# Optimization experiments

Measured on AMD Instinct MI355X. Metric: run time of the kernel, lower is better.

## Reference

```python
import jax, jax.numpy as jnp
import numpy as np

D, LEN_IN, LEN_OUT = 2, 1, 10
H1, H2 = 32, 32
B, T = 4096, 512
F_IN = D * LEN_IN          # 2
F_OUT = D * LEN_OUT        # 20


def setup_inputs() -> dict:
    key = jax.random.key(0)
    ks = jax.random.split(key, 12)
    s = 1.0 / np.sqrt(H1)  # PyTorch default init scale for LSTMCell/Linear
    u = lambda k, shape: jax.random.uniform(k, shape, jnp.float32, -s, s)
    return {
        "x": jax.random.normal(ks[0], (B, T, F_IN), jnp.float32),
        # LSTMCell 1 (input 2 -> hidden 32); gate order i,f,g,o stacked on dim 0
        "W_ih1": u(ks[1], (4 * H1, F_IN)),
        "W_hh1": u(ks[2], (4 * H1, H1)),
        "b_ih1": u(ks[3], (4 * H1,)),
        "b_hh1": u(ks[4], (4 * H1,)),
        # LSTMCell 2 (32 -> 32)
        "W_ih2": u(ks[5], (4 * H2, H1)),
        "W_hh2": u(ks[6], (4 * H2, H2)),
        "b_ih2": u(ks[7], (4 * H2,)),
        "b_hh2": u(ks[8], (4 * H2,)),
        # Final linear 32 -> 20
        "W_out": u(ks[9], (F_OUT, H2)),
        "b_out": u(ks[10], (F_OUT,)),
    }


def _lstm_cell(x, h, c, W_ih, W_hh, b):
    # gates: [B, 4H]; PyTorch gate order i, f, g, o
    gates = x @ W_ih.T + h @ W_hh.T + b
    i, f, g, o = jnp.split(gates, 4, axis=-1)
    i, f, o = jax.nn.sigmoid(i), jax.nn.sigmoid(f), jax.nn.sigmoid(o)
    g = jnp.tanh(g)
    c_new = f * c + i * g
    h_new = o * jnp.tanh(c_new)
    return h_new, c_new


def reference(x, W_ih1, W_hh1, b_ih1, b_hh1, W_ih2, W_hh2, b_ih2, b_hh2, W_out, b_out):
    b1 = b_ih1 + b_hh1
    b2 = b_ih2 + b_hh2
    Bsz = x.shape[0]
    h1 = jnp.zeros((Bsz, H1), x.dtype)
    c1 = jnp.zeros((Bsz, H1), x.dtype)
    h2 = jnp.zeros((Bsz, H2), x.dtype)
    c2 = jnp.zeros((Bsz, H2), x.dtype)

    def step(carry, x_t):
        h1, c1, h2, c2 = carry
        h1, c1 = _lstm_cell(x_t, h1, c1, W_ih1, W_hh1, b1)
        h2, c2 = _lstm_cell(h1, h2, c2, W_ih2, W_hh2, b2)
        out_t = h2 @ W_out.T + b_out  # [B, 20]
        return (h1, c1, h2, c2), out_t

    xs = jnp.swapaxes(x, 0, 1)  # [T, B, F_IN]
    _, outs = jax.lax.scan(step, (h1, c1, h2, c2), xs)  # outs: [T, B, 20]
    outs = jnp.swapaxes(outs, 0, 1)  # [B, T, 20]
    return outs.reshape(Bsz, x.shape[1], D, LEN_OUT)
```

## Files before the change

### kernel.cpp

```cpp
#include <hip/hip_runtime.h>
#include <hip/hip_fp16.h>

#define TLEN 512
#define HDIM 32
#define FOUT 20
#define HST  36

typedef __attribute__((ext_vector_type(8))) short bf16x8;
typedef __attribute__((ext_vector_type(4))) float f32x4;
typedef __attribute__((ext_vector_type(4))) short s16x4;

__device__ __forceinline__ float sigm(float v) {
  float e = __builtin_amdgcn_exp2f(-1.4426950408889634f * v);
  return __builtin_amdgcn_rcpf(1.0f + e);
}
__device__ __forceinline__ float tanh_f(float v) {
  float e = __builtin_amdgcn_exp2f(2.8853900817779268f * v);
  return 1.0f - 2.0f * __builtin_amdgcn_rcpf(1.0f + e);
}
__device__ __forceinline__ void hilo(float v, short& h, short& l) {
  unsigned u = __builtin_bit_cast(unsigned, v);
  unsigned r = u + 0x7fffu + ((u >> 16) & 1u);
  h = (short)(r >> 16);
  float hf = __builtin_bit_cast(float, r & 0xffff0000u);
  float res = v - hf;
  unsigned u2 = __builtin_bit_cast(unsigned, res);
  unsigned r2 = u2 + 0x7fffu + ((u2 >> 16) & 1u);
  l = (short)(r2 >> 16);
}

__device__ __forceinline__ void barrier_lgkm() {
  asm volatile("s_waitcnt lgkmcnt(0)\n\ts_barrier" ::: "memory");
}

__device__ __forceinline__ bf16x8 read_h(const short* buf, int off) {
  s16x4 a = *(const s16x4*)(buf + off);
  s16x4 b = *(const s16x4*)(buf + off + 4);
  bf16x8 r;
  r[0]=a[0]; r[1]=a[1]; r[2]=a[2]; r[3]=a[3];
  r[4]=b[0]; r[5]=b[1]; r[6]=b[2]; r[7]=b[3];
  return r;
}

__device__ __forceinline__ float lstm_update(const f32x4& g, float& c) {
  float iv = sigm(g[0]), fv = sigm(g[1]), gv = tanh_f(g[2]), ov = sigm(g[3]);
  c = fv * c + iv * gv;
  return ov * tanh_f(c);
}

__global__ __launch_bounds__(512, 2) void lstm_seq_kernel(
    const float* __restrict__ xg,
    const float* __restrict__ Wih1, const float* __restrict__ Whh1,
    const float* __restrict__ bih1, const float* __restrict__ bhh1,
    const float* __restrict__ Wih2, const float* __restrict__ Whh2,
    const float* __restrict__ bih2, const float* __restrict__ bhh2,
    const float* __restrict__ Wout, const float* __restrict__ bout,
    float* __restrict__ out)
{
  __shared__ __half xl[16 * 1028];
  __shared__ short h1hiB[2][16 * HST], h1loB[2][16 * HST];
  __shared__ short h2hiB[2][16 * HST], h2loB[2][16 * HST];

  const int tid  = threadIdx.x;
  const int w    = tid >> 6;
  const int lane = tid & 63;
  const int n    = lane & 15;
  const int q    = lane >> 4;
  const int q4   = q * 4;
  const int q8   = q * 8;
  const int b0   = blockIdx.x * 16;
  const int p    = w & 1;

  for (int idx = tid; idx < 16 * 1024; idx += 512) {
    int row = idx >> 10, col = idx & 1023;
    xl[row * 1028 + col] = __float2half(xg[((size_t)(b0 + row) << 10) + col]);
  }

  const int og = (n & 3) * HDIM + 4 * w + (n >> 2);
  bf16x8 Whh1h, Whh1l, Wih2h, Wih2l, Whh2h, Whh2l;
  #pragma unroll
  for (int j = 0; j < 8; j++) {
    short hh, ll;
    hilo(Whh1[og * HDIM + q8 + j], hh, ll); Whh1h[j] = hh; Whh1l[j] = ll;
    hilo(Wih2[og * HDIM + q8 + j], hh, ll); Wih2h[j] = hh; Wih2l[j] = ll;
    hilo(Whh2[og * HDIM + q8 + j], hh, ll); Whh2h[j] = hh; Whh2l[j] = ll;
  }
  float b1c[4], b2c[4], wx0[4], wx1[4], boc[4];
  #pragma unroll
  for (int r = 0; r < 4; r++) {
    int gr = r * HDIM + 4 * w + q;
    b1c[r] = bih1[gr] + bhh1[gr];
    b2c[r] = bih2[gr] + bhh2[gr];
    wx0[r] = Wih1[gr * 2 + 0];
    wx1[r] = Wih1[gr * 2 + 1];
    int orow = 16 * p + q4 + r;
    boc[r] = (orow < FOUT) ? bout[orow] : 0.0f;
  }
  bf16x8 WoH = {0,0,0,0,0,0,0,0}, WoL = {0,0,0,0,0,0,0,0};
  {
    int orow = 16 * p + n;
    if (orow < FOUT) {
      #pragma unroll
      for (int j = 0; j < 8; j++) {
        short hh, ll;
        hilo(Wout[orow * HDIM + q8 + j], hh, ll); WoH[j] = hh; WoL[j] = ll;
      }
    }
  }

  const int hoff = n * HST + 4 * w + q;
  const int aoff = n * HST + q8;
  float c1 = 0.0f, c2 = 0.0f;

  bf16x8 h1h = {0,0,0,0,0,0,0,0}, h1l = {0,0,0,0,0,0,0,0};
  bf16x8 h2h = {0,0,0,0,0,0,0,0}, h2l = {0,0,0,0,0,0,0,0};

  __syncthreads();

  {
    __half2 hv = *(const __half2*)&xl[n * 1028];
    float xv0 = __half2float(hv.x), xv1 = __half2float(hv.y);
    f32x4 g1;
    #pragma unroll
    for (int r = 0; r < 4; r++) g1[r] = fmaf(xv1, wx1[r], fmaf(xv0, wx0[r], b1c[r]));
    float h1n = lstm_update(g1, c1);
    short hh, ll; hilo(h1n, hh, ll);
    h1hiB[0][hoff] = hh; h1loB[0][hoff] = ll;
    barrier_lgkm();
    h1h = read_h(h1hiB[0], aoff);
    h1l = read_h(h1loB[0], aoff);
  }

  for (int t = 1; t < TLEN; ++t) {
    const int par = t & 1;
    __half2 hv = *(const __half2*)&xl[n * 1028 + 2 * t];
    float xv0 = __half2float(hv.x), xv1 = __half2float(hv.y);

    f32x4 g1;
    #pragma unroll
    for (int r = 0; r < 4; r++) g1[r] = fmaf(xv1, wx1[r], fmaf(xv0, wx0[r], b1c[r]));
    g1 = __builtin_amdgcn_mfma_f32_16x16x32_bf16(Whh1h, h1h, g1, 0, 0, 0);
    g1 = __builtin_amdgcn_mfma_f32_16x16x32_bf16(Whh1l, h1h, g1, 0, 0, 0);
    g1 = __builtin_amdgcn_mfma_f32_16x16x32_bf16(Whh1h, h1l, g1, 0, 0, 0);

    f32x4 ga, gb;
    #pragma unroll
    for (int r = 0; r < 4; r++) { ga[r] = b2c[r]; gb[r] = 0.0f; }
    ga = __builtin_amdgcn_mfma_f32_16x16x32_bf16(Wih2h, h1h, ga, 0, 0, 0);
    gb = __builtin_amdgcn_mfma_f32_16x16x32_bf16(Whh2h, h2h, gb, 0, 0, 0);
    ga = __builtin_amdgcn_mfma_f32_16x16x32_bf16(Wih2l, h1h, ga, 0, 0, 0);
    gb = __builtin_amdgcn_mfma_f32_16x16x32_bf16(Whh2l, h2h, gb, 0, 0, 0);
    ga = __builtin_amdgcn_mfma_f32_16x16x32_bf16(Wih2h, h1l, ga, 0, 0, 0);
    gb = __builtin_amdgcn_mfma_f32_16x16x32_bf16(Whh2h, h2l, gb, 0, 0, 0);

    float h1n = lstm_update(g1, c1);
    f32x4 g2;
    #pragma unroll
    for (int r = 0; r < 4; r++) g2[r] = ga[r] + gb[r];
    float h2n = lstm_update(g2, c2);

    short hh, ll;
    hilo(h1n, hh, ll); h1hiB[par][hoff] = hh; h1loB[par][hoff] = ll;
    hilo(h2n, hh, ll); h2hiB[par][hoff] = hh; h2loB[par][hoff] = ll;

    barrier_lgkm();

    h1h = read_h(h1hiB[par], aoff);
    h1l = read_h(h1loB[par], aoff);
    h2h = read_h(h2hiB[par], aoff);
    h2l = read_h(h2loB[par], aoff);

    const int s = t - 1;
    if ((w >> 1) == (s & 3)) {
      f32x4 ao;
      #pragma unroll
      for (int r = 0; r < 4; r++) ao[r] = boc[r];
      ao = __builtin_amdgcn_mfma_f32_16x16x32_bf16(WoH, h2h, ao, 0, 0, 0);
      ao = __builtin_amdgcn_mfma_f32_16x16x32_bf16(WoL, h2h, ao, 0, 0, 0);
      ao = __builtin_amdgcn_mfma_f32_16x16x32_bf16(WoH, h2l, ao, 0, 0, 0);
      if (p == 0 || q == 0) {
        float4 st = { ao[0], ao[1], ao[2], ao[3] };
        *(float4*)&out[((size_t)(b0 + n) * TLEN + s) * FOUT + 16 * p + q4] = st;
      }
    }
  }

  {
    f32x4 ga, gb;
    #pragma unroll
    for (int r = 0; r < 4; r++) { ga[r] = b2c[r]; gb[r] = 0.0f; }
    ga = __builtin_amdgcn_mfma_f32_16x16x32_bf16(Wih2h, h1h, ga, 0, 0, 0);
    gb = __builtin_amdgcn_mfma_f32_16x16x32_bf16(Whh2h, h2h, gb, 0, 0, 0);
    ga = __builtin_amdgcn_mfma_f32_16x16x32_bf16(Wih2l, h1h, ga, 0, 0, 0);
    gb = __builtin_amdgcn_mfma_f32_16x16x32_bf16(Whh2l, h2h, gb, 0, 0, 0);
    ga = __builtin_amdgcn_mfma_f32_16x16x32_bf16(Wih2h, h1l, ga, 0, 0, 0);
    gb = __builtin_amdgcn_mfma_f32_16x16x32_bf16(Whh2h, h2l, gb, 0, 0, 0);
    f32x4 g2;
    #pragma unroll
    for (int r = 0; r < 4; r++) g2[r] = ga[r] + gb[r];
    float h2n = lstm_update(g2, c2);
    short hh, ll; hilo(h2n, hh, ll);
    h2hiB[0][hoff] = hh; h2loB[0][hoff] = ll;
    barrier_lgkm();
    h2h = read_h(h2hiB[0], aoff);
    h2l = read_h(h2loB[0], aoff);
    const int s = TLEN - 1;
    if ((w >> 1) == (s & 3)) {
      f32x4 ao;
      #pragma unroll
      for (int r = 0; r < 4; r++) ao[r] = boc[r];
      ao = __builtin_amdgcn_mfma_f32_16x16x32_bf16(WoH, h2h, ao, 0, 0, 0);
      ao = __builtin_amdgcn_mfma_f32_16x16x32_bf16(WoL, h2h, ao, 0, 0, 0);
      ao = __builtin_amdgcn_mfma_f32_16x16x32_bf16(WoH, h2l, ao, 0, 0, 0);
      if (p == 0 || q == 0) {
        float4 st = { ao[0], ao[1], ao[2], ao[3] };
        *(float4*)&out[((size_t)(b0 + n) * TLEN + s) * FOUT + 16 * p + q4] = st;
      }
    }
  }
}

extern "C" void kernel_launch(void* const* d_in, const int* in_sizes, int n_in,
                              void* d_out, int out_size, void* d_ws, size_t ws_size,
                              hipStream_t stream) {
  const float* xg   = (const float*)d_in[0];
  const float* Wih1 = (const float*)d_in[1];
  const float* Whh1 = (const float*)d_in[2];
  const float* bih1 = (const float*)d_in[3];
  const float* bhh1 = (const float*)d_in[4];
  const float* Wih2 = (const float*)d_in[5];
  const float* Whh2 = (const float*)d_in[6];
  const float* bih2 = (const float*)d_in[7];
  const float* bhh2 = (const float*)d_in[8];
  const float* Wout = (const float*)d_in[9];
  const float* bout = (const float*)d_in[10];
  float* out = (float*)d_out;

  hipLaunchKernelGGL(lstm_seq_kernel, dim3(256), dim3(512), 0, stream,
                     xg, Wih1, Whh1, bih1, bhh1, Wih2, Whh2, bih2, bhh2, Wout, bout, out);
}
```

Baseline: 500.1 us.

## Split LSTM layers across separate wavefront groups in a 1024-thread block

Doubles the block to 16 wavefronts: waves 0-7 compute layer 1 and the output projection, waves 8-15 compute layer 2, each holding only its own layer's weights. The per-step critical path per wave shrinks to a single layer's MFMAs and gate math, and the output projection now lags by one extra step and runs on the layer-1 waves. The trade-off is that every step's barrier now synchronises 1024 threads, and occupancy per CU drops to one block instead of two.

Result: no change. 494.3 us (-1.2%).

```diff
diff --git a/kernel.cpp b/kernel.cpp
--- a/kernel.cpp
+++ b/kernel.cpp
@@ -48,7 +48,7 @@
   return ov * tanh_f(c);
 }
 
-__global__ __launch_bounds__(512, 2) void lstm_seq_kernel(
+__global__ __launch_bounds__(1024, 1) void lstm_seq_kernel(
     const float* __restrict__ xg,
     const float* __restrict__ Wih1, const float* __restrict__ Whh1,
     const float* __restrict__ bih1, const float* __restrict__ bhh1,
@@ -69,35 +69,35 @@
   const int q4   = q * 4;
   const int q8   = q * 8;
   const int b0   = blockIdx.x * 16;
+  const bool isL1 = (w < 8);
+  const int wr   = w & 7;
   const int p    = w & 1;
-
-  for (int idx = tid; idx < 16 * 1024; idx += 512) {
+  const int pr   = w >> 1;
+
+  for (int idx = tid; idx < 16 * 1024; idx += 1024) {
     int row = idx >> 10, col = idx & 1023;
     xl[row * 1028 + col] = __float2half(xg[((size_t)(b0 + row) << 10) + col]);
   }
 
-  const int og = (n & 3) * HDIM + 4 * w + (n >> 2);
-  bf16x8 Whh1h, Whh1l, Wih2h, Wih2l, Whh2h, Whh2l;
-  #pragma unroll
-  for (int j = 0; j < 8; j++) {
-    short hh, ll;
-    hilo(Whh1[og * HDIM + q8 + j], hh, ll); Whh1h[j] = hh; Whh1l[j] = ll;
-    hilo(Wih2[og * HDIM + q8 + j], hh, ll); Wih2h[j] = hh; Wih2l[j] = ll;
-    hilo(Whh2[og * HDIM + q8 + j], hh, ll); Whh2h[j] = hh; Whh2l[j] = ll;
-  }
-  float b1c[4], b2c[4], wx0[4], wx1[4], boc[4];
-  #pragma unroll
-  for (int r = 0; r < 4; r++) {
-    int gr = r * HDIM + 4 * w + q;
-    b1c[r] = bih1[gr] + bhh1[gr];
-    b2c[r] = bih2[gr] + bhh2[gr];
-    wx0[r] = Wih1[gr * 2 + 0];
-    wx1[r] = Wih1[gr * 2 + 1];
-    int orow = 16 * p + q4 + r;
-    boc[r] = (orow < FOUT) ? bout[orow] : 0.0f;
-  }
+  const int og = (n & 3) * HDIM + 4 * wr + (n >> 2);
+  bf16x8 WAh, WAl, WBh, WBl;
+  float bc[4], wx0[4], wx1[4], boc[4];
   bf16x8 WoH = {0,0,0,0,0,0,0,0}, WoL = {0,0,0,0,0,0,0,0};
-  {
+  if (isL1) {
+    #pragma unroll
+    for (int j = 0; j < 8; j++) {
+      short hh, ll;
+      hilo(Whh1[og * HDIM + q8 + j], hh, ll); WAh[j] = hh; WAl[j] = ll;
+    }
+    #pragma unroll
+    for (int r = 0; r < 4; r++) {
+      int gr = r * HDIM + 4 * wr + q;
+      bc[r]  = bih1[gr] + bhh1[gr];
+      wx0[r] = Wih1[gr * 2 + 0];
+      wx1[r] = Wih1[gr * 2 + 1];
+      int orow = 16 * p + q4 + r;
+      boc[r] = (orow < FOUT) ? bout[orow] : 0.0f;
+    }
     int orow = 16 * p + n;
     if (orow < FOUT) {
       #pragma unroll
@@ -106,116 +106,146 @@
         hilo(Wout[orow * HDIM + q8 + j], hh, ll); WoH[j] = hh; WoL[j] = ll;
       }
     }
-  }
-
-  const int hoff = n * HST + 4 * w + q;
+  } else {
+    #pragma unroll
+    for (int j = 0; j < 8; j++) {
+      short hh, ll;
+      hilo(Wih2[og * HDIM + q8 + j], hh, ll); WAh[j] = hh; WAl[j] = ll;
+      hilo(Whh2[og * HDIM + q8 + j], hh, ll); WBh[j] = hh; WBl[j] = ll;
+    }
+    #pragma unroll
+    for (int r = 0; r < 4; r++) {
+      int gr = r * HDIM + 4 * wr + q;
+      bc[r] = bih2[gr] + bhh2[gr];
+    }
+  }
+
+  const int hoff = n * HST + 4 * wr + q;
   const int aoff = n * HST + q8;
-  float c1 = 0.0f, c2 = 0.0f;
+  float c = 0.0f;
 
   bf16x8 h1h = {0,0,0,0,0,0,0,0}, h1l = {0,0,0,0,0,0,0,0};
   bf16x8 h2h = {0,0,0,0,0,0,0,0}, h2l = {0,0,0,0,0,0,0,0};
 
   __syncthreads();
 
-  {
+  if (isL1) {
     __half2 hv = *(const __half2*)&xl[n * 1028];
     float xv0 = __half2float(hv.x), xv1 = __half2float(hv.y);
     f32x4 g1;
     #pragma unroll
-    for (int r = 0; r < 4; r++) g1[r] = fmaf(xv1, wx1[r], fmaf(xv0, wx0[r], b1c[r]));
-    float h1n = lstm_update(g1, c1);
+    for (int r = 0; r < 4; r++) g1[r] = fmaf(xv1, wx1[r], fmaf(xv0, wx0[r], bc[r]));
+    float h1n = lstm_update(g1, c);
     short hh, ll; hilo(h1n, hh, ll);
     h1hiB[0][hoff] = hh; h1loB[0][hoff] = ll;
-    barrier_lgkm();
-    h1h = read_h(h1hiB[0], aoff);
-    h1l = read_h(h1loB[0], aoff);
-  }
+  }
+  barrier_lgkm();
+  h1h = read_h(h1hiB[0], aoff);
+  h1l = read_h(h1loB[0], aoff);
 
   for (int t = 1; t < TLEN; ++t) {
     const int par = t & 1;
-    __half2 hv = *(const __half2*)&xl[n * 1028 + 2 * t];
-    float xv0 = __half2float(hv.x), xv1 = __half2float(hv.y);
-
-    f32x4 g1;
-    #pragma unroll
-    for (int r = 0; r < 4; r++) g1[r] = fmaf(xv1, wx1[r], fmaf(xv0, wx0[r], b1c[r]));
-    g1 = __builtin_amdgcn_mfma_f32_16x16x32_bf16(Whh1h, h1h, g1, 0, 0, 0);
-    g1 = __builtin_amdgcn_mfma_f32_16x16x32_bf16(Whh1l, h1h, g1, 0, 0, 0);
-    g1 = __builtin_amdgcn_mfma_f32_16x16x32_bf16(Whh1h, h1l, g1, 0, 0, 0);
-
-    f32x4 ga, gb;
-    #pragma unroll
-    for (int r = 0; r < 4; r++) { ga[r] = b2c[r]; gb[r] = 0.0f; }
-    ga = __builtin_amdgcn_mfma_f32_16x16x32_bf16(Wih2h, h1h, ga, 0, 0, 0);
-    gb = __builtin_amdgcn_mfma_f32_16x16x32_bf16(Whh2h, h2h, gb, 0, 0, 0);
-    ga = __builtin_amdgcn_mfma_f32_16x16x32_bf16(Wih2l, h1h, ga, 0, 0, 0);
-    gb = __builtin_amdgcn_mfma_f32_16x16x32_bf16(Whh2l, h2h, gb, 0, 0, 0);
-    ga = __builtin_amdgcn_mfma_f32_16x16x32_bf16(Wih2h, h1l, ga, 0, 0, 0);
-    gb = __builtin_amdgcn_mfma_f32_16x16x32_bf16(Whh2h, h2l, gb, 0, 0, 0);
-
-    float h1n = lstm_update(g1, c1);
-    f32x4 g2;
-    #pragma unroll
-    for (int r = 0; r < 4; r++) g2[r] = ga[r] + gb[r];
-    float h2n = lstm_update(g2, c2);
-
-    short hh, ll;
-    hilo(h1n, hh, ll); h1hiB[par][hoff] = hh; h1loB[par][hoff] = ll;
-    hilo(h2n, hh, ll); h2hiB[par][hoff] = hh; h2loB[par][hoff] = ll;
+    if (isL1) {
+      __half2 hv = *(const __half2*)&xl[n * 1028 + 2 * t];
+      float xv0 = __half2float(hv.x), xv1 = __half2float(hv.y);
+
+      f32x4 g1;
+      #pragma unroll
+      for (int r = 0; r < 4; r++) g1[r] = fmaf(xv1, wx1[r], fmaf(xv0, wx0[r], bc[r]));
+      g1 = __builtin_amdgcn_mfma_f32_16x16x32_bf16(WAh, h1h, g1, 0, 0, 0);
+      g1 = __builtin_amdgcn_mfma_f32_16x16x32_bf16(WAl, h1h, g1, 0, 0, 0);
+      g1 = __builtin_amdgcn_mfma_f32_16x16x32_bf16(WAh, h1l, g1, 0, 0, 0);
+
+      float h1n = lstm_update(g1, c);
+      short hh, ll; hilo(h1n, hh, ll);
+      h1hiB[par][hoff] = hh; h1loB[par][hoff] = ll;
+
+      const int s = t - 2;
+      if (s >= 0 && pr == (s & 3)) {
+        f32x4 ao;
+        #pragma unroll
+        for (int r = 0; r < 4; r++) ao[r] = boc[r];
+        ao = __builtin_amdgcn_mfma_f32_16x16x32_bf16(WoH, h2h, ao, 0, 0, 0);
+        ao = __builtin_amdgcn_mfma_f32_16x16x32_bf16(WoL, h2h, ao, 0, 0, 0);
+        ao = __builtin_amdgcn_mfma_f32_16x16x32_bf16(WoH, h2l, ao, 0, 0, 0);
+        if (p == 0 || q == 0) {
+          float4 st = { ao[0], ao[1], ao[2], ao[3] };
+          *(float4*)&out[((size_t)(b0 + n) * TLEN + s) * FOUT + 16 * p + q4] = st;
+        }
+      }
+    } else {
+      f32x4 ga, gb;
+      #pragma unroll
+      for (int r = 0; r < 4; r++) { ga[r] = bc[r]; gb[r] = 0.0f; }
+      ga = __builtin_amdgcn_mfma_f32_16x16x32_bf16(WAh, h1h, ga, 0, 0, 0);
+      gb = __builtin_amdgcn_mfma_f32_16x16x32_bf16(WBh, h2h, gb, 0, 0, 0);
+      ga = __builtin_amdgcn_mfma_f32_16x16x32_bf16(WAl, h1h, ga, 0, 0, 0);
+      gb = __builtin_amdgcn_mfma_f32_16x16x32_bf16(WBl, h2h, gb, 0, 0, 0);
+      ga = __builtin_amdgcn_mfma_f32_16x16x32_bf16(WAh, h1l, ga, 0, 0, 0);
+      gb = __builtin_amdgcn_mfma_f32_16x16x32_bf16(WBh, h2l, gb, 0, 0, 0);
+
+      f32x4 g2;
+      #pragma unroll
+      for (int r = 0; r < 4; r++) g2[r] = ga[r] + gb[r];
+      float h2n = lstm_update(g2, c);
+      short hh, ll; hilo(h2n, hh, ll);
+      h2hiB[par][hoff] = hh; h2loB[par][hoff] = ll;
+    }
 
     barrier_lgkm();
 
     h1h = read_h(h1hiB[par], aoff);
     h1l = read_h(h1loB[par], aoff);
-    h2h = read_h(h2hiB[par], aoff);
-    h2l = read_h(h2loB[par], aoff);
-
-    const int s = t - 1;
-    if ((w >> 1) == (s & 3)) {
-      f32x4 ao;
-      #pragma unroll
-      for (int r = 0; r < 4; r++) ao[r] = boc[r];
-      ao = __builtin_amdgcn_mfma_f32_16x16x32_bf16(WoH, h2h, ao, 0, 0, 0);
-      ao = __builtin_amdgcn_mfma_f32_16x16x32_bf16(WoL, h2h, ao, 0, 0, 0);
-      ao = __builtin_amdgcn_mfma_f32_16x16x32_bf16(WoH, h2l, ao, 0, 0, 0);
-      if (p == 0 || q == 0) {
-        float4 st = { ao[0], ao[1], ao[2], ao[3] };
-        *(float4*)&out[((size_t)(b0 + n) * TLEN + s) * FOUT + 16 * p + q4] = st;
-      }
-    }
-  }
-
-  {
+    if (!isL1 || pr == ((t - 1) & 3)) {
+      h2h = read_h(h2hiB[par], aoff);
+      h2l = read_h(h2loB[par], aoff);
+    }
+  }
+
+  if (!isL1) {
     f32x4 ga, gb;
     #pragma unroll
-    for (int r = 0; r < 4; r++) { ga[r] = b2c[r]; gb[r] = 0.0f; }
-    ga = __builtin_amdgcn_mfma_f32_16x16x32_bf16(Wih2h, h1h, ga, 0, 0, 0);
-    gb = __builtin_amdgcn_mfma_f32_16x16x32_bf16(Whh2h, h2h, gb, 0, 0, 0);
-    ga = __builtin_amdgcn_mfma_f32_16x16x32_bf16(Wih2l, h1h, ga, 0, 0, 0);
-    gb = __builtin_amdgcn_mfma_f32_16x16x32_bf16(Whh2l, h2h, gb, 0, 0, 0);
-    ga = __builtin_amdgcn_mfma_f32_16x16x32_bf16(Wih2h, h1l, ga, 0, 0, 0);
-    gb = __builtin_amdgcn_mfma_f32_16x16x32_bf16(Whh2h, h2l, gb, 0, 0, 0);
+    for (int r = 0; r < 4; r++) { ga[r] = bc[r]; gb[r] = 0.0f; }
+    ga = __builtin_amdgcn_mfma_f32_16x16x32_bf16(WAh, h1h, ga, 0, 0, 0);
+    gb = __builtin_amdgcn_mfma_f32_16x16x32_bf16(WBh, h2h, gb, 0, 0, 0);
+    ga = __builtin_amdgcn_mfma_f32_16x16x32_bf16(WAl, h1h, ga, 0, 0, 0);
+    gb = __builtin_amdgcn_mfma_f32_16x16x32_bf16(WBl, h2h, gb, 0, 0, 0);
+    ga = __builtin_amdgcn_mfma_f32_16x16x32_bf16(WAh, h1l, ga, 0, 0, 0);
+    gb = __builtin_amdgcn_mfma_f32_16x16x32_bf16(WBh, h2l, gb, 0, 0, 0);
     f32x4 g2;
     #pragma unroll
     for (int r = 0; r < 4; r++) g2[r] = ga[r] + gb[r];
-    float h2n = lstm_update(g2, c2);
+    float h2n = lstm_update(g2, c);
     short hh, ll; hilo(h2n, hh, ll);
     h2hiB[0][hoff] = hh; h2loB[0][hoff] = ll;
-    barrier_lgkm();
+  } else if (pr == 2) {
+    const int s = TLEN - 2;
+    f32x4 ao;
+    #pragma unroll
+    for (int r = 0; r < 4; r++) ao[r] = boc[r];
+    ao = __builtin_amdgcn_mfma_f32_16x16x32_bf16(WoH, h2h, ao, 0, 0, 0);
+    ao = __builtin_amdgcn_mfma_f32_16x16x32_bf16(WoL, h2h, ao, 0, 0, 0);
+    ao = __builtin_amdgcn_mfma_f32_16x16x32_bf16(WoH, h2l, ao, 0, 0, 0);
+    if (p == 0 || q == 0) {
+      float4 st = { ao[0], ao[1], ao[2], ao[3] };
+      *(float4*)&out[((size_t)(b0 + n) * TLEN + s) * FOUT + 16 * p + q4] = st;
+    }
+  }
+  barrier_lgkm();
+
+  if (isL1 && pr == 3) {
     h2h = read_h(h2hiB[0], aoff);
     h2l = read_h(h2loB[0], aoff);
     const int s = TLEN - 1;
-    if ((w >> 1) == (s & 3)) {
-      f32x4 ao;
-      #pragma unroll
-      for (int r = 0; r < 4; r++) ao[r] = boc[r];
-      ao = __builtin_amdgcn_mfma_f32_16x16x32_bf16(WoH, h2h, ao, 0, 0, 0);
-      ao = __builtin_amdgcn_mfma_f32_16x16x32_bf16(WoL, h2h, ao, 0, 0, 0);
-      ao = __builtin_amdgcn_mfma_f32_16x16x32_bf16(WoH, h2l, ao, 0, 0, 0);
-      if (p == 0 || q == 0) {
-        float4 st = { ao[0], ao[1], ao[2], ao[3] };
-        *(float4*)&out[((size_t)(b0 + n) * TLEN + s) * FOUT + 16 * p + q4] = st;
-      }
+    f32x4 ao;
+    #pragma unroll
+    for (int r = 0; r < 4; r++) ao[r] = boc[r];
+    ao = __builtin_amdgcn_mfma_f32_16x16x32_bf16(WoH, h2h, ao, 0, 0, 0);
+    ao = __builtin_amdgcn_mfma_f32_16x16x32_bf16(WoL, h2h, ao, 0, 0, 0);
+    ao = __builtin_amdgcn_mfma_f32_16x16x32_bf16(WoH, h2l, ao, 0, 0, 0);
+    if (p == 0 || q == 0) {
+      float4 st = { ao[0], ao[1], ao[2], ao[3] };
+      *(float4*)&out[((size_t)(b0 + n) * TLEN + s) * FOUT + 16 * p + q4] = st;
     }
   }
 }
@@ -236,6 +266,6 @@
   const float* bout = (const float*)d_in[10];
   float* out = (float*)d_out;
 
-  hipLaunchKernelGGL(lstm_seq_kernel, dim3(256), dim3(512), 0, stream,
+  hipLaunchKernelGGL(lstm_seq_kernel, dim3(256), dim3(1024), 0, stream,
                      xg, Wih1, Whh1, bih1, bhh1, Wih2, Whh2, bih2, bhh2, Wout, bout, out);
 }
```
